# Kernel optimization log

Measured on AMD Instinct MI355X. Metric: run time of the kernel, lower is better.

The kernel has to match this reference:

```python
import jax, jax.numpy as jnp
import numpy as np

H, W = 480, 640
FLOW_SCALING = float(max(H, W))  # config default: max(resolution)
REGUL_WEIGHT = 0.001
MAX_TS = 1.0  # single association pass
EPS = 1e-9


def setup_inputs() -> dict:
    key = jax.random.key(0)
    k1, k2, k3, k4, k5 = jax.random.split(key, 5)
    B, N = 8, 131072
    # scale flow so warped displacements (flow * flow_scaling) are O(tens of px)
    flow = jax.random.normal(k1, (B, 2, H, W), jnp.float32) * 0.05
    ts = jax.random.uniform(k2, (B, N, 1), dtype=jnp.float32)
    ys = jax.random.randint(k3, (B, N), 0, H, dtype=jnp.int32)
    xs = jax.random.randint(k4, (B, N), 0, W, dtype=jnp.int32)
    pol = jax.random.randint(k5, (B, N), 0, 2, dtype=jnp.int32)  # 1 = positive event
    return {"flow": flow, "ts": ts, "ys": ys, "xs": xs, "pol": pol}


def _get_interpolation(ys, xs, ts0, fy, fx, tref):
    """Warp events to tref and build bilinear splat indices/weights.
    ys/xs: [B,N] int; ts0: [B,N] float; fy/fx: per-event flow [B,N].
    Returns idx [B,4N] int32 (flattened y*W+x) and weights [B,4N]."""
    dt = tref - ts0
    wy = ys.astype(jnp.float32) + dt * fy * FLOW_SCALING  # warped y [B,N]
    wx = xs.astype(jnp.float32) + dt * fx * FLOW_SCALING  # warped x [B,N]
    ty = jnp.floor(wy)
    by = ty + 1.0
    lx = jnp.floor(wx)
    rx = lx + 1.0
    # corner order: top-left, top-right, bottom-left, bottom-right -> [B,4N]
    iy = jnp.concatenate([ty, ty, by, by], axis=1)
    ix = jnp.concatenate([lx, rx, lx, rx], axis=1)
    wy4 = jnp.tile(wy, (1, 4))
    wx4 = jnp.tile(wx, (1, 4))
    w = jnp.maximum(0.0, 1.0 - jnp.abs(wy4 - iy)) * jnp.maximum(0.0, 1.0 - jnp.abs(wx4 - ix))
    inb = (iy >= 0) & (iy < H) & (ix >= 0) & (ix < W)
    iy = jnp.where(inb, iy, 0.0)
    ix = jnp.where(inb, ix, 0.0)
    w = w * inb.astype(w.dtype)
    idx = (iy * W + ix).astype(jnp.int32)
    return idx, w


def _splat(idx, w):
    """Scatter-add weights into per-pixel image. idx,w: [B,4N] -> [B,H*W]."""
    B = idx.shape[0]
    out = jnp.zeros((B, H * W), dtype=w.dtype)
    return out.at[jnp.arange(B)[:, None], idx].add(w)


def reference(flow, ts, ys, xs, pol):
    B, N = ys.shape
    # gather per-event flow (x channel 0, y channel 1) at original event pixels
    flat = ys * W + xs  # [B,N]
    flow_flat = flow.reshape(B, 2, H * W)
    bidx = jnp.arange(B)[:, None]
    fx = flow_flat[bidx, 0, flat]
    fy = flow_flat[bidx, 1, flat]

    ts0 = ts[..., 0]
    ts4 = jnp.tile(ts0, (1, 4))
    pos4 = jnp.tile(pol.astype(jnp.float32), (1, 4))
    neg4 = 1.0 - pos4

    def iwe_loss(tref, ts_w):
        idx, w = _get_interpolation(ys, xs, ts0, fy, fx, tref)
        iwe_pos = _splat(idx, w * pos4)
        iwe_neg = _splat(idx, w * neg4)
        iwe_pos_ts = _splat(idx, w * ts_w * pos4) / (iwe_pos + EPS) / MAX_TS
        iwe_neg_ts = _splat(idx, w * ts_w * neg4) / (iwe_neg + EPS) / MAX_TS
        l = jnp.sum(iwe_pos_ts ** 2, axis=1) + jnp.sum(iwe_neg_ts ** 2, axis=1)
        nz = jnp.sum(((iwe_pos + iwe_neg) > 0).astype(l.dtype), axis=1)
        return jnp.sum(l / nz)

    fw_loss = iwe_loss(MAX_TS, ts4)
    bw_loss = iwe_loss(0.0, MAX_TS - ts4)

    # flow smoothness (charbonnier over 4 spatial directions)
    fxm = flow[:, 0:1]
    fym = flow[:, 1:2]
    charb = lambda a, b: jnp.sqrt(a * a + b * b + 1e-6)
    dx = charb(fxm[..., :, :-1] - fxm[..., :, 1:], fym[..., :, :-1] - fym[..., :, 1:])
    dy = charb(fxm[..., :-1, :] - fxm[..., 1:, :], fym[..., :-1, :] - fym[..., 1:, :])
    dr = charb(fxm[..., :-1, :-1] - fxm[..., 1:, 1:], fym[..., :-1, :-1] - fym[..., 1:, 1:])
    ur = charb(fxm[..., 1:, :-1] - fxm[..., :-1, 1:], fym[..., 1:, :-1] - fym[..., :-1, 1:])
    smooth = (jnp.mean(dx) + jnp.mean(dy) + jnp.mean(dr) + jnp.mean(ur)) / 4.0

    return fw_loss + bw_loss + REGUL_WEIGHT * smooth
```

## Files before the change

kernel.cpp:

```cpp
#include <hip/hip_runtime.h>


constexpr int H = 480, W = 640, HW = H * W;
constexpr int B = 8, N = 131072;
constexpr float FLOW_SCALING = 640.0f;
constexpr float EPS = 1e-9f;

constexpr int TH = 48, TW = 64;
constexpr int TILES_Y = H / TH;
constexpr int TILES_X = W / TW;
constexpr int TILES = TILES_Y * TILES_X;
constexpr int NBINS = B * 2 * TILES;
constexpr int CAP = 4096;

constexpr float PSCALE = 262144.0f;
constexpr float PINV = 1.0f / 262144.0f;

constexpr int BND_BLK = 44;
constexpr int SM_BLK = 512;
constexpr int SC_BLOCKS = 1024;

constexpr int BPX = TILES_Y * W + TILES_X * H;

constexpr size_t ACCL_OFF = 0;
constexpr size_t ACCN_OFF = ACCL_OFF + (size_t)16 * TILES * 8;
constexpr size_t BNDL_OFF = ACCN_OFF + (size_t)16 * TILES * 8;
constexpr size_t BNDN_OFF = BNDL_OFF + (size_t)16 * BND_BLK * 8;
constexpr size_t SMP_OFF  = BNDN_OFF + (size_t)16 * BND_BLK * 8;
constexpr size_t CUR_OFF  = SMP_OFF + (size_t)SM_BLK * 4 * 8;
constexpr size_t BND_OFF  = CUR_OFF + (size_t)NBINS * 4;
constexpr size_t BND_BYTES = (size_t)16 * BPX * 2 * 8;
constexpr size_t ITEMS_OFF = BND_OFF + BND_BYTES;

__device__ inline double blk_reduce(double v, double* sm) {
    __syncthreads();
    #pragma unroll
    for (int o = 32; o > 0; o >>= 1) v += __shfl_down(v, o, 64);
    int lane = threadIdx.x & 63;
    int wid  = threadIdx.x >> 6;
    if (lane == 0) sm[wid] = v;
    __syncthreads();
    double r = 0.0;
    if (threadIdx.x == 0) {
        int nw = (int)(blockDim.x >> 6);
        for (int w2 = 0; w2 < nw; ++w2) r += sm[w2];
    }
    return r;
}

__device__ inline int bin_from_payload(unsigned long long v) {
    int t = (int)(v & 1);
    int fyi = (int)((unsigned)(v >> 40) >> 12) - 512;
    int fxi = (int)(((unsigned)(v >> 16) & 0xFFFFFFu) >> 12) - 512;
    int cy = min(max(fyi, 0), H - 1);
    int cx = min(max(fxi, 0), W - 1);
    return t * TILES + (cy / TH) * TILES_X + (cx >> 6);
}

__global__ __launch_bounds__(256) void scatter_kernel(
    const float* __restrict__ flow, const float* __restrict__ ts,
    const int* __restrict__ ys, const int* __restrict__ xs,
    const int* __restrict__ pol,
    unsigned long long* __restrict__ items, unsigned* __restrict__ cursors) {
    __shared__ unsigned scount[200];
    __shared__ unsigned sbase[200];
    __shared__ unsigned scur[200];
    int tid = threadIdx.x;
    if (tid < 200) { scount[tid] = 0; scur[tid] = 0; }
    __syncthreads();

    int b = blockIdx.x & 7;
    int chunk = blockIdx.x >> 3;
    int e0 = b * N + chunk * 1024;
    const float* fb = flow + (size_t)b * 2 * HW;

    unsigned long long pay[8];
    #pragma unroll
    for (int k = 0; k < 4; ++k) {
        int e = e0 + k * 256 + tid;
        int y = ys[e], x = xs[e], p = pol[e];
        float t0 = ts[e];
        int flat = y * W + x;
        float fx = fb[flat];
        float fy = fb[HW + flat];
        #pragma unroll
        for (int t = 0; t < 2; ++t) {
            float dt = (t == 0 ? 1.0f : 0.0f) - t0;
            float sw = (t == 0) ? t0 : 1.0f - t0;
            float wy = (float)y + dt * fy * FLOW_SCALING;
            float wx = (float)x + dt * fx * FLOW_SCALING;
            unsigned long long v = ~0ull;
            if (wy >= -1.0f && wy < (float)H && wx >= -1.0f && wx < (float)W) {
                unsigned uy = __float2uint_rn((wy + 512.0f) * 4096.0f);
                unsigned ux = __float2uint_rn((wx + 512.0f) * 4096.0f);
                unsigned usw = __float2uint_rn(sw * 16383.0f);
                v = ((unsigned long long)uy << 40) |
                    ((unsigned long long)ux << 16) |
                    ((unsigned long long)usw << 2) |
                    ((unsigned long long)(p != 0) << 1) |
                    (unsigned long long)t;
                atomicAdd(&scount[bin_from_payload(v)], 1u);
            }
            pay[k * 2 + t] = v;
        }
    }
    __syncthreads();
    if (tid < 200) {
        unsigned c = scount[tid];
        sbase[tid] = c ? atomicAdd(&cursors[b * 200 + tid], c) : 0u;
    }
    __syncthreads();
    #pragma unroll
    for (int i = 0; i < 8; ++i) {
        unsigned long long v = pay[i];
        if (v == ~0ull) continue;
        int binl = bin_from_payload(v);
        unsigned idx = sbase[binl] + atomicAdd(&scur[binl], 1u);
        if (idx < (unsigned)CAP)
            items[(size_t)(b * 200 + binl) * CAP + idx] = v;
    }
}

__global__ __launch_bounds__(256) void accum_kernel(
    const unsigned long long* __restrict__ items,
    const unsigned* __restrict__ cursors,
    unsigned long long* __restrict__ bnd,
    double* __restrict__ accL, double* __restrict__ accN) {
    constexpr int TPX = (TH + 1) * (TW + 1);
    __shared__ unsigned long long sacc[2 * TPX];
    __shared__ double sm[8];
    int tid = threadIdx.x;
    for (int i = tid; i < 2 * TPX; i += 256) sacc[i] = 0ull;
    __syncthreads();

    int bin = blockIdx.x;
    int b = bin / 200;
    int loc = bin - b * 200;
    int t = loc / TILES;
    int tile = loc - t * TILES;
    int y0 = (tile / TILES_X) * TH;
    int x0 = (tile % TILES_X) * TW;
    int cnt = (int)min(cursors[bin], (unsigned)CAP);
    const unsigned long long* bi = items + (size_t)bin * CAP;

    for (int i = tid; i < cnt; i += 256) {
        unsigned long long v = bi[i];
        unsigned uy = (unsigned)(v >> 40);
        unsigned ux = (unsigned)(v >> 16) & 0xFFFFFFu;
        float wy = (float)uy * (1.0f / 4096.0f) - 512.0f;
        float wx = (float)ux * (1.0f / 4096.0f) - 512.0f;
        int fyi = (int)(uy >> 12) - 512;
        int fxi = (int)(ux >> 12) - 512;
        float sw = (float)((unsigned)(v >> 2) & 0x3FFFu) * (1.0f / 16383.0f);
        int f = ((v >> 1) & 1) ? 0 : 1;
        #pragma unroll
        for (int dy = 0; dy < 2; ++dy) {
            int ry = fyi + dy, ly = ry - y0;
            if (ry < 0 || ry >= H || ly < 0 || ly > TH) continue;
            float wfy = 1.0f - fabsf(wy - (float)ry);
            #pragma unroll
            for (int dx = 0; dx < 2; ++dx) {
                int rx = fxi + dx, lx = rx - x0;
                if (rx < 0 || rx >= W || lx < 0 || lx > TW) continue;
                float wgt = wfy * (1.0f - fabsf(wx - (float)rx));
                int px = ly * (TW + 1) + lx;
                unsigned w18 = __float2uint_rn(wgt * PSCALE);
                unsigned s18 = __float2uint_rn(wgt * sw * PSCALE);
                atomicAdd(&sacc[f * TPX + px],
                          ((unsigned long long)w18 << 32) | s18);
            }
        }
    }
    __syncthreads();

    double l = 0.0, nz = 0.0;
    unsigned long long* bj = bnd + (size_t)(b * 2 + t) * BPX * 2;
    for (int p = tid; p < TPX; p += 256) {
        int ly = p / (TW + 1), lx = p - ly * (TW + 1);
        int y = y0 + ly, x = x0 + lx;
        if (y >= H || x >= W) continue;
        unsigned long long vp = sacc[p];
        unsigned long long vn = sacc[TPX + p];
        if (ly == 0 || ly == TH) {
            int off = (y / TH) * W + x;
            if (vp) atomicAdd(&bj[(size_t)off * 2], vp);
            if (vn) atomicAdd(&bj[(size_t)off * 2 + 1], vn);
        } else if (lx == 0 || lx == TW) {
            int off = TILES_Y * W + (x >> 6) * H + y;
            if (vp) atomicAdd(&bj[(size_t)off * 2], vp);
            if (vn) atomicAdd(&bj[(size_t)off * 2 + 1], vn);
        } else {
            float fwp = (float)(unsigned)(vp >> 32) * PINV;
            float fsp = (float)(unsigned)vp * PINV;
            float fwn = (float)(unsigned)(vn >> 32) * PINV;
            float fsn = (float)(unsigned)vn * PINV;
            float a = fsp / (fwp + EPS);
            float c = fsn / (fwn + EPS);
            l += (double)(a * a + c * c);
            if ((vp | vn) >> 32) nz += 1.0;
        }
    }
    double lt = blk_reduce(l, sm);
    double nt = blk_reduce(nz, sm);
    if (tid == 0) {
        int j = b * 2 + t;
        accL[j * TILES + tile] = lt;
        accN[j * TILES + tile] = nt;
    }
}

__global__ __launch_bounds__(256) void bound_kernel(
    const unsigned long long* __restrict__ bnd,
    double* __restrict__ bndL, double* __restrict__ bndN) {
    __shared__ double sm[8];
    int j = blockIdx.y;
    double l = 0.0, nz = 0.0;
    for (int p = blockIdx.x * blockDim.x + threadIdx.x; p < BPX;
         p += gridDim.x * blockDim.x) {
        unsigned long long vp = bnd[((size_t)j * BPX + p) * 2];
        unsigned long long vn = bnd[((size_t)j * BPX + p) * 2 + 1];
        unsigned wp = (unsigned)(vp >> 32), sp = (unsigned)vp;
        unsigned wn = (unsigned)(vn >> 32), sn = (unsigned)vn;
        float a = ((float)sp * PINV) / ((float)wp * PINV + EPS);
        float c = ((float)sn * PINV) / ((float)wn * PINV + EPS);
        l += (double)(a * a + c * c);
        if (wp | wn) nz += 1.0;
    }
    double lt = blk_reduce(l, sm);
    double nt = blk_reduce(nz, sm);
    if (threadIdx.x == 0) {
        bndL[j * BND_BLK + blockIdx.x] = lt;
        bndN[j * BND_BLK + blockIdx.x] = nt;
    }
}

__device__ inline float charb(float a, float b) {
    return sqrtf(a * a + b * b + 1e-6f);
}

__global__ __launch_bounds__(256) void smooth_kernel(
    const float* __restrict__ flow, double* __restrict__ smP) {
    __shared__ double sm[8];
    double sdx = 0.0, sdy = 0.0, sdr = 0.0, sur = 0.0;
    int stride = gridDim.x * blockDim.x;
    for (int i = blockIdx.x * blockDim.x + threadIdx.x; i < B * HW; i += stride) {
        int b = i / HW;
        int rem = i - b * HW;
        int y = rem / W;
        int x = rem - y * W;
        const float* fx = flow + (size_t)(b * 2 + 0) * HW;
        const float* fy = flow + (size_t)(b * 2 + 1) * HW;
        float f00 = fx[rem], g00 = fy[rem];
        bool xe = (x + 1) < W;
        bool ye = (y + 1) < H;
        if (xe) {
            float f01 = fx[rem + 1], g01 = fy[rem + 1];
            sdx += (double)charb(f00 - f01, g00 - g01);
            if (ye) {
                float f10 = fx[rem + W], g10 = fy[rem + W];
                float f11 = fx[rem + W + 1], g11 = fy[rem + W + 1];
                sdy += (double)charb(f00 - f10, g00 - g10);
                sdr += (double)charb(f00 - f11, g00 - g11);
                sur += (double)charb(f10 - f01, g10 - g01);
            }
        } else if (ye) {
            float f10 = fx[rem + W], g10 = fy[rem + W];
            sdy += (double)charb(f00 - f10, g00 - g10);
        }
    }
    double tt;
    tt = blk_reduce(sdx, sm); if (threadIdx.x == 0) smP[blockIdx.x * 4 + 0] = tt;
    tt = blk_reduce(sdy, sm); if (threadIdx.x == 0) smP[blockIdx.x * 4 + 1] = tt;
    tt = blk_reduce(sdr, sm); if (threadIdx.x == 0) smP[blockIdx.x * 4 + 2] = tt;
    tt = blk_reduce(sur, sm); if (threadIdx.x == 0) smP[blockIdx.x * 4 + 3] = tt;
}

__global__ __launch_bounds__(256) void final_kernel(
    const double* __restrict__ accL, const double* __restrict__ accN,
    const double* __restrict__ bndL, const double* __restrict__ bndN,
    const double* __restrict__ smP, float* __restrict__ out) {
    __shared__ double sj[16];
    __shared__ double sm[8];
    int tid = threadIdx.x;
    int j = tid >> 4, s = tid & 15;
    double l = 0.0, nz = 0.0;
    for (int i = s; i < TILES; i += 16) {
        l += accL[j * TILES + i];
        nz += accN[j * TILES + i];
    }
    for (int i = s; i < BND_BLK; i += 16) {
        l += bndL[j * BND_BLK + i];
        nz += bndN[j * BND_BLK + i];
    }
    #pragma unroll
    for (int o = 8; o > 0; o >>= 1) {
        l += __shfl_down(l, o, 16);
        nz += __shfl_down(nz, o, 16);
    }
    if (s == 0) sj[j] = l / nz;

    double c[4] = {0.0, 0.0, 0.0, 0.0};
    for (int i = tid; i < SM_BLK; i += 256) {
        #pragma unroll
        for (int k = 0; k < 4; ++k) c[k] += smP[i * 4 + k];
    }
    double s0 = blk_reduce(c[0], sm);
    double s1 = blk_reduce(c[1], sm);
    double s2 = blk_reduce(c[2], sm);
    double s3 = blk_reduce(c[3], sm);
    __syncthreads();
    if (tid == 0) {
        double loss = 0.0;
        for (int q = 0; q < 16; ++q) loss += sj[q];
        double ndx = (double)B * H * (W - 1);
        double ndy = (double)B * (H - 1) * W;
        double ndd = (double)B * (H - 1) * (W - 1);
        double smooth = (s0 / ndx + s1 / ndy + s2 / ndd + s3 / ndd) * 0.25;
        out[0] = (float)(loss + 0.001 * smooth);
    }
}

extern "C" void kernel_launch(void* const* d_in, const int* in_sizes, int n_in,
                              void* d_out, int out_size, void* d_ws, size_t ws_size,
                              hipStream_t stream) {
    const float* flow = (const float*)d_in[0];
    const float* ts   = (const float*)d_in[1];
    const int*   ys   = (const int*)d_in[2];
    const int*   xs   = (const int*)d_in[3];
    const int*   pol  = (const int*)d_in[4];
    float* out = (float*)d_out;

    char* ws = (char*)d_ws;
    double* accL = (double*)(ws + ACCL_OFF);
    double* accN = (double*)(ws + ACCN_OFF);
    double* bndL = (double*)(ws + BNDL_OFF);
    double* bndN = (double*)(ws + BNDN_OFF);
    double* smP  = (double*)(ws + SMP_OFF);
    unsigned* cursors = (unsigned*)(ws + CUR_OFF);
    unsigned long long* bnd = (unsigned long long*)(ws + BND_OFF);
    unsigned long long* items = (unsigned long long*)(ws + ITEMS_OFF);

    hipMemsetAsync(ws + CUR_OFF, 0, ITEMS_OFF - CUR_OFF, stream);
    smooth_kernel<<<SM_BLK, 256, 0, stream>>>(flow, smP);
    scatter_kernel<<<SC_BLOCKS, 256, 0, stream>>>(flow, ts, ys, xs, pol, items, cursors);
    accum_kernel<<<NBINS, 256, 0, stream>>>(items, cursors, bnd, accL, accN);
    bound_kernel<<<dim3(BND_BLK, 16), 256, 0, stream>>>(bnd, bndL, bndN);
    final_kernel<<<1, 256, 0, stream>>>(accL, accN, bndL, bndN, smP, out);
}
```

Measured before the change: 159.0 us.

## Fuse smoothness into scatter launch and store tile edges without global atomics

Merges the smoothness reduction kernel into the scatter kernel as extra blocks, which removes one launch and lets the two run concurrently. Each accumulation tile now writes its halo and edge pixels to a private per-tile edge buffer with plain stores instead of 64-bit global atomics into a shared boundary image. The bound kernel then sums the up-to-four overlapping tile contributions per boundary pixel. Because every edge slot is overwritten each call, the large boundary-buffer memset shrinks to clearing only the cursors. The cost is more complex index math and extra gathered reads in the bound kernel.

New measurement: 154.2 us. 1.03x faster.

```diff
diff --git a/kernel.cpp b/kernel.cpp
--- a/kernel.cpp
+++ b/kernel.cpp
@@ -20,6 +20,8 @@
 constexpr int SM_BLK = 512;
 constexpr int SC_BLOCKS = 1024;
 
+constexpr int EDGE_PX = 224;
+
 constexpr int BPX = TILES_Y * W + TILES_X * H;
 
 constexpr size_t ACCL_OFF = 0;
@@ -28,9 +30,9 @@
 constexpr size_t BNDN_OFF = BNDL_OFF + (size_t)16 * BND_BLK * 8;
 constexpr size_t SMP_OFF  = BNDN_OFF + (size_t)16 * BND_BLK * 8;
 constexpr size_t CUR_OFF  = SMP_OFF + (size_t)SM_BLK * 4 * 8;
-constexpr size_t BND_OFF  = CUR_OFF + (size_t)NBINS * 4;
-constexpr size_t BND_BYTES = (size_t)16 * BPX * 2 * 8;
-constexpr size_t ITEMS_OFF = BND_OFF + BND_BYTES;
+constexpr size_t BNDE_OFF = CUR_OFF + (size_t)NBINS * 4;
+constexpr size_t BNDE_BYTES = (size_t)NBINS * EDGE_PX * 2 * 8;
+constexpr size_t ITEMS_OFF = BNDE_OFF + BNDE_BYTES;
 
 __device__ inline double blk_reduce(double v, double* sm) {
     __syncthreads();
@@ -57,15 +59,59 @@
     return t * TILES + (cy / TH) * TILES_X + (cx >> 6);
 }
 
-__global__ __launch_bounds__(256) void scatter_kernel(
+__device__ inline float charb(float a, float b) {
+    return sqrtf(a * a + b * b + 1e-6f);
+}
+
+__global__ __launch_bounds__(256) void scatter_smooth_kernel(
     const float* __restrict__ flow, const float* __restrict__ ts,
     const int* __restrict__ ys, const int* __restrict__ xs,
     const int* __restrict__ pol,
-    unsigned long long* __restrict__ items, unsigned* __restrict__ cursors) {
+    unsigned long long* __restrict__ items, unsigned* __restrict__ cursors,
+    double* __restrict__ smP) {
     __shared__ unsigned scount[200];
     __shared__ unsigned sbase[200];
     __shared__ unsigned scur[200];
+    __shared__ double sm[8];
     int tid = threadIdx.x;
+
+    if (blockIdx.x >= SC_BLOCKS) {
+        int sb = blockIdx.x - SC_BLOCKS;
+        double sdx = 0.0, sdy = 0.0, sdr = 0.0, sur = 0.0;
+        int stride = SM_BLK * 256;
+        for (int i = sb * 256 + tid; i < B * HW; i += stride) {
+            int b = i / HW;
+            int rem = i - b * HW;
+            int y = rem / W;
+            int x = rem - y * W;
+            const float* fx = flow + (size_t)(b * 2 + 0) * HW;
+            const float* fy = flow + (size_t)(b * 2 + 1) * HW;
+            float f00 = fx[rem], g00 = fy[rem];
+            bool xe = (x + 1) < W;
+            bool ye = (y + 1) < H;
+            if (xe) {
+                float f01 = fx[rem + 1], g01 = fy[rem + 1];
+                sdx += (double)charb(f00 - f01, g00 - g01);
+                if (ye) {
+                    float f10 = fx[rem + W], g10 = fy[rem + W];
+                    float f11 = fx[rem + W + 1], g11 = fy[rem + W + 1];
+                    sdy += (double)charb(f00 - f10, g00 - g10);
+                    sdr += (double)charb(f00 - f11, g00 - g11);
+                    sur += (double)charb(f10 - f01, g10 - g01);
+                }
+            } else if (ye) {
+                float f10 = fx[rem + W], g10 = fy[rem + W];
+                sdy += (double)charb(f00 - f10, g00 - g10);
+            }
+        }
+        double tt;
+        tt = blk_reduce(sdx, sm); if (tid == 0) smP[sb * 4 + 0] = tt;
+        tt = blk_reduce(sdy, sm); if (tid == 0) smP[sb * 4 + 1] = tt;
+        tt = blk_reduce(sdr, sm); if (tid == 0) smP[sb * 4 + 2] = tt;
+        tt = blk_reduce(sur, sm); if (tid == 0) smP[sb * 4 + 3] = tt;
+        return;
+    }
+
     if (tid < 200) { scount[tid] = 0; scur[tid] = 0; }
     __syncthreads();
 
@@ -124,7 +170,7 @@
 __global__ __launch_bounds__(256) void accum_kernel(
     const unsigned long long* __restrict__ items,
     const unsigned* __restrict__ cursors,
-    unsigned long long* __restrict__ bnd,
+    unsigned long long* __restrict__ bndE,
     double* __restrict__ accL, double* __restrict__ accN) {
     constexpr int TPX = (TH + 1) * (TW + 1);
     __shared__ unsigned long long sacc[2 * TPX];
@@ -174,21 +220,19 @@
     __syncthreads();
 
     double l = 0.0, nz = 0.0;
-    unsigned long long* bj = bnd + (size_t)(b * 2 + t) * BPX * 2;
+    unsigned long long* eb = bndE + (size_t)bin * EDGE_PX * 2;
     for (int p = tid; p < TPX; p += 256) {
         int ly = p / (TW + 1), lx = p - ly * (TW + 1);
-        int y = y0 + ly, x = x0 + lx;
-        if (y >= H || x >= W) continue;
         unsigned long long vp = sacc[p];
         unsigned long long vn = sacc[TPX + p];
-        if (ly == 0 || ly == TH) {
-            int off = (y / TH) * W + x;
-            if (vp) atomicAdd(&bj[(size_t)off * 2], vp);
-            if (vn) atomicAdd(&bj[(size_t)off * 2 + 1], vn);
-        } else if (lx == 0 || lx == TW) {
-            int off = TILES_Y * W + (x >> 6) * H + y;
-            if (vp) atomicAdd(&bj[(size_t)off * 2], vp);
-            if (vn) atomicAdd(&bj[(size_t)off * 2 + 1], vn);
+        int slot = -1;
+        if (ly == 0)           slot = lx;
+        else if (ly == TH)     slot = 65 + lx;
+        else if (lx == 0)      slot = 130 + (ly - 1);
+        else if (lx == TW)     slot = 177 + (ly - 1);
+        if (slot >= 0) {
+            eb[(size_t)slot * 2]     = vp;
+            eb[(size_t)slot * 2 + 1] = vn;
         } else {
             float fwp = (float)(unsigned)(vp >> 32) * PINV;
             float fsp = (float)(unsigned)vp * PINV;
@@ -210,15 +254,50 @@
 }
 
 __global__ __launch_bounds__(256) void bound_kernel(
-    const unsigned long long* __restrict__ bnd,
+    const unsigned long long* __restrict__ bndE,
     double* __restrict__ bndL, double* __restrict__ bndN) {
     __shared__ double sm[8];
     int j = blockIdx.y;
+    int b = j >> 1, t = j & 1;
+    const unsigned long long* jb =
+        bndE + (size_t)(b * 200 + t * 100) * EDGE_PX * 2;
+
     double l = 0.0, nz = 0.0;
     for (int p = blockIdx.x * blockDim.x + threadIdx.x; p < BPX;
          p += gridDim.x * blockDim.x) {
-        unsigned long long vp = bnd[((size_t)j * BPX + p) * 2];
-        unsigned long long vn = bnd[((size_t)j * BPX + p) * 2 + 1];
+        unsigned long long vp = 0ull, vn = 0ull;
+        if (p < TILES_Y * W) {
+            int k = p / W, x = p - k * W;
+            int m = x >> 6, lx = x & 63;
+            const unsigned long long* e;
+            e = jb + ((size_t)(k * TILES_X + m) * EDGE_PX + lx) * 2;
+            vp += e[0]; vn += e[1];
+            if (k > 0) {
+                e = jb + ((size_t)((k - 1) * TILES_X + m) * EDGE_PX + 65 + lx) * 2;
+                vp += e[0]; vn += e[1];
+            }
+            if (lx == 0 && m > 0) {
+                e = jb + ((size_t)(k * TILES_X + m - 1) * EDGE_PX + 64) * 2;
+                vp += e[0]; vn += e[1];
+                if (k > 0) {
+                    e = jb + ((size_t)((k - 1) * TILES_X + m - 1) * EDGE_PX + 129) * 2;
+                    vp += e[0]; vn += e[1];
+                }
+            }
+        } else {
+            int q = p - TILES_Y * W;
+            int m = q / H, y = q - m * H;
+            int r = y / TH, ly = y - r * TH;
+            if (ly != 0) {
+                const unsigned long long* e;
+                e = jb + ((size_t)(r * TILES_X + m) * EDGE_PX + 130 + ly - 1) * 2;
+                vp += e[0]; vn += e[1];
+                if (m > 0) {
+                    e = jb + ((size_t)(r * TILES_X + m - 1) * EDGE_PX + 177 + ly - 1) * 2;
+                    vp += e[0]; vn += e[1];
+                }
+            }
+        }
         unsigned wp = (unsigned)(vp >> 32), sp = (unsigned)vp;
         unsigned wn = (unsigned)(vn >> 32), sn = (unsigned)vn;
         float a = ((float)sp * PINV) / ((float)wp * PINV + EPS);
@@ -232,47 +311,6 @@
         bndL[j * BND_BLK + blockIdx.x] = lt;
         bndN[j * BND_BLK + blockIdx.x] = nt;
     }
-}
-
-__device__ inline float charb(float a, float b) {
-    return sqrtf(a * a + b * b + 1e-6f);
-}
-
-__global__ __launch_bounds__(256) void smooth_kernel(
-    const float* __restrict__ flow, double* __restrict__ smP) {
-    __shared__ double sm[8];
-    double sdx = 0.0, sdy = 0.0, sdr = 0.0, sur = 0.0;
-    int stride = gridDim.x * blockDim.x;
-    for (int i = blockIdx.x * blockDim.x + threadIdx.x; i < B * HW; i += stride) {
-        int b = i / HW;
-        int rem = i - b * HW;
-        int y = rem / W;
-        int x = rem - y * W;
-        const float* fx = flow + (size_t)(b * 2 + 0) * HW;
-        const float* fy = flow + (size_t)(b * 2 + 1) * HW;
-        float f00 = fx[rem], g00 = fy[rem];
-        bool xe = (x + 1) < W;
-        bool ye = (y + 1) < H;
-        if (xe) {
-            float f01 = fx[rem + 1], g01 = fy[rem + 1];
-            sdx += (double)charb(f00 - f01, g00 - g01);
-            if (ye) {
-                float f10 = fx[rem + W], g10 = fy[rem + W];
-                float f11 = fx[rem + W + 1], g11 = fy[rem + W + 1];
-                sdy += (double)charb(f00 - f10, g00 - g10);
-                sdr += (double)charb(f00 - f11, g00 - g11);
-                sur += (double)charb(f10 - f01, g10 - g01);
-            }
-        } else if (ye) {
-            float f10 = fx[rem + W], g10 = fy[rem + W];
-            sdy += (double)charb(f00 - f10, g00 - g10);
-        }
-    }
-    double tt;
-    tt = blk_reduce(sdx, sm); if (threadIdx.x == 0) smP[blockIdx.x * 4 + 0] = tt;
-    tt = blk_reduce(sdy, sm); if (threadIdx.x == 0) smP[blockIdx.x * 4 + 1] = tt;
-    tt = blk_reduce(sdr, sm); if (threadIdx.x == 0) smP[blockIdx.x * 4 + 2] = tt;
-    tt = blk_reduce(sur, sm); if (threadIdx.x == 0) smP[blockIdx.x * 4 + 3] = tt;
 }
 
 __global__ __launch_bounds__(256) void final_kernel(
@@ -337,13 +375,13 @@
     double* bndN = (double*)(ws + BNDN_OFF);
     double* smP  = (double*)(ws + SMP_OFF);
     unsigned* cursors = (unsigned*)(ws + CUR_OFF);
-    unsigned long long* bnd = (unsigned long long*)(ws + BND_OFF);
+    unsigned long long* bndE = (unsigned long long*)(ws + BNDE_OFF);
     unsigned long long* items = (unsigned long long*)(ws + ITEMS_OFF);
 
-    hipMemsetAsync(ws + CUR_OFF, 0, ITEMS_OFF - CUR_OFF, stream);
-    smooth_kernel<<<SM_BLK, 256, 0, stream>>>(flow, smP);
-    scatter_kernel<<<SC_BLOCKS, 256, 0, stream>>>(flow, ts, ys, xs, pol, items, cursors);
-    accum_kernel<<<NBINS, 256, 0, stream>>>(items, cursors, bnd, accL, accN);
-    bound_kernel<<<dim3(BND_BLK, 16), 256, 0, stream>>>(bnd, bndL, bndN);
+    hipMemsetAsync(cursors, 0, (size_t)NBINS * 4, stream);
+    scatter_smooth_kernel<<<SC_BLOCKS + SM_BLK, 256, 0, stream>>>(
+        flow, ts, ys, xs, pol, items, cursors, smP);
+    accum_kernel<<<NBINS, 256, 0, stream>>>(items, cursors, bndE, accL, accN);
+    bound_kernel<<<dim3(BND_BLK, 16), 256, 0, stream>>>(bndE, bndL, bndN);
     final_kernel<<<1, 256, 0, stream>>>(accL, accN, bndL, bndN, smP, out);
 }
```
